# Performance work log

Hardware: AMD Instinct MI355X
Metric: run time of the kernel (lower is better)

Reference implementation:

```python
import jax, jax.numpy as jnp
import numpy as np

N_NODES = 100000


def _gcn_norm(src, dst, n_nodes, n_edges):
    # PyG gcn_norm with add_self_loops=False: deg over target (col) index
    ones = jnp.ones((n_edges,), dtype=jnp.float32)
    deg = jax.ops.segment_sum(ones, dst, num_segments=n_nodes)
    dinv = jnp.where(deg > 0, jax.lax.rsqrt(deg), 0.0)
    return dinv[src] * dinv[dst]  # [E]


def _arma_conv(x, src, dst, ew, init_w, root_w, bias, n_nodes):
    # x: [N, Fin]; init_w/root_w: [K, Fin, Fout]; bias: [K, 1, Fout]
    h = jnp.einsum('nf,kfo->kno', x, init_w)          # [K, N, Fout]
    msg = h[:, src, :] * ew[None, :, None]             # [K, E, Fout]
    agg = jax.vmap(lambda m: jax.ops.segment_sum(m, dst, num_segments=n_nodes))(msg)
    out = agg + jnp.einsum('nf,kfo->kno', x, root_w) + bias
    return jax.nn.relu(out).mean(axis=0)               # mean over stacks K


def setup_inputs() -> dict:
    key = jax.random.key(0)
    ks = jax.random.split(key, 8)
    n, e = N_NODES, 3200000
    nfeat, hid, nclass, K = 512, 16, 40, 2
    x = jax.random.normal(ks[0], (n, nfeat), dtype=jnp.float32)
    edge_index = jax.random.randint(ks[1], (2, e), 0, n, dtype=jnp.int32)
    s1 = (1.0 / np.sqrt(nfeat)).astype(np.float32) if isinstance(np.sqrt(nfeat), np.ndarray) else np.float32(1.0 / np.sqrt(nfeat))
    s2 = np.float32(1.0 / np.sqrt(hid))
    iw1 = jax.random.normal(ks[2], (K, nfeat, hid), dtype=jnp.float32) * s1
    rw1 = jax.random.normal(ks[3], (K, nfeat, hid), dtype=jnp.float32) * s1
    b1 = jax.random.normal(ks[4], (K, 1, hid), dtype=jnp.float32) * 0.01
    iw2 = jax.random.normal(ks[5], (K, hid, nclass), dtype=jnp.float32) * s2
    rw2 = jax.random.normal(ks[6], (K, hid, nclass), dtype=jnp.float32) * s2
    b2 = jax.random.normal(ks[7], (K, 1, nclass), dtype=jnp.float32) * 0.01
    return {'x': x, 'edge_index': edge_index, 'iw1': iw1, 'rw1': rw1, 'b1': b1,
            'iw2': iw2, 'rw2': rw2, 'b2': b2}


def reference(x, edge_index, iw1, rw1, b1, iw2, rw2, b2):
    src, dst = edge_index[0], edge_index[1]
    n = N_NODES
    ew = _gcn_norm(src, dst, n, src.shape[0])
    h = _arma_conv(x, src, dst, ew, iw1, rw1, b1, n)   # [N, 16]
    out = _arma_conv(h, src, dst, ew, iw2, rw2, b2, n) # [N, nclass]
    return out
```

## Files before the change

kernel.cpp:

```cpp
#include <hip/hip_runtime.h>


#define TB 256
#define CHA 4096

typedef __attribute__((ext_vector_type(8))) short bf8;
typedef __attribute__((ext_vector_type(4))) float f4;

__device__ inline unsigned short f2bf_rne(float f) {
  unsigned int u = __float_as_uint(f);
  unsigned int r = u + 0x7fffu + ((u >> 16) & 1u);
  return (unsigned short)(r >> 16);
}
__device__ inline float bf2f(unsigned short h) {
  return __uint_as_float(((unsigned int)h) << 16);
}
__device__ inline float bflo(unsigned int u) { return __uint_as_float(u << 16); }
__device__ inline float bfhi(unsigned int u) { return __uint_as_float(u & 0xffff0000u); }
__device__ inline unsigned int bfpack(float lo, float hi) {
  return (unsigned int)f2bf_rne(lo) | ((unsigned int)f2bf_rne(hi) << 16);
}

#define ACC8(v)                                   \
  do {                                            \
    a[0] += bflo((v).x); a[1] += bfhi((v).x);     \
    a[2] += bflo((v).y); a[3] += bfhi((v).y);     \
    a[4] += bflo((v).z); a[5] += bfhi((v).z);     \
    a[6] += bflo((v).w); a[7] += bfhi((v).w);     \
  } while (0)

#define ACC4(v)                                   \
  do {                                            \
    a[0] += bflo((v).x); a[1] += bfhi((v).x);     \
    a[2] += bflo((v).y); a[3] += bfhi((v).y);     \
  } while (0)

__global__ __launch_bounds__(256) void k_init(int* __restrict__ ccur, int cap) {
  ccur[threadIdx.x] = threadIdx.x * cap;
}

__global__ __launch_bounds__(TB) void k_binA(const int* __restrict__ src,
                                             const int* __restrict__ dst,
                                             int* __restrict__ ccur,
                                             unsigned int* __restrict__ epairs,
                                             int E) {
  __shared__ int cnt[256];
  __shared__ int gb[256];
  int tid = threadIdx.x;
  cnt[tid] = 0;
  __syncthreads();
  int e0 = blockIdx.x * CHA;
  int e1 = min(e0 + CHA, E);
  for (int e = e0 + tid; e < e1; e += TB) atomicAdd(&cnt[dst[e] >> 9], 1);
  __syncthreads();
  int c = cnt[tid];
  if (c > 0) gb[tid] = atomicAdd(&ccur[tid], c);
  __syncthreads();
  cnt[tid] = 0;
  __syncthreads();
  for (int e = e0 + tid; e < e1; e += TB) {
    int dv = dst[e];
    int b = dv >> 9;
    int r = atomicAdd(&cnt[b], 1);
    epairs[gb[b] + r] = ((unsigned int)src[e] << 9) | (unsigned int)(dv & 511);
  }
}

__global__ __launch_bounds__(TB) void k_binB(const unsigned int* __restrict__ epairs,
                                             const int* __restrict__ ccur,
                                             int* __restrict__ degi,
                                             int* __restrict__ offsets,
                                             int* __restrict__ srcs,
                                             float* __restrict__ dinv,
                                             int N, int cap, int scap) {
  __shared__ int cnt[512];
  __shared__ int pre[512];
  int b = blockIdx.x;
  int n0 = b << 9;
  int tid = threadIdx.x;
  int beg = b * cap;
  int end = ccur[b];
  int pbase = b * scap;
  int i0 = tid, i1 = tid + 256;
  cnt[i0] = 0; cnt[i1] = 0;
  __syncthreads();
  for (int e = beg + tid; e < end; e += TB)
    atomicAdd(&cnt[epairs[e] & 511u], 1);
  __syncthreads();
  int pd0 = (cnt[i0] + 7) & ~7;
  int pd1 = (cnt[i1] + 7) & ~7;
  pre[i0] = pd0; pre[i1] = pd1;
  __syncthreads();
  for (int d = 1; d < 512; d <<= 1) {
    int t0 = (i0 >= d) ? pre[i0 - d] : 0;
    int t1 = (i1 >= d) ? pre[i1 - d] : 0;
    __syncthreads();
    pre[i0] += t0; pre[i1] += t1;
    __syncthreads();
  }
  int s0 = pre[i0] - pd0;
  int s1 = pre[i1] - pd1;
  if (n0 + i0 < N) {
    int c0 = cnt[i0];
    degi[n0 + i0] = c0;
    offsets[n0 + i0] = pbase + s0;
    dinv[n0 + i0] = c0 > 0 ? rsqrtf((float)c0) : 0.0f;
  }
  if (n0 + i1 < N) {
    int c1 = cnt[i1];
    degi[n0 + i1] = c1;
    offsets[n0 + i1] = pbase + s1;
    dinv[n0 + i1] = c1 > 0 ? rsqrtf((float)c1) : 0.0f;
  }
  __syncthreads();
  cnt[i0] = s0; cnt[i1] = s1;
  __syncthreads();
  for (int e = beg + tid; e < end; e += TB) {
    unsigned int p = epairs[e];
    int pos = atomicAdd(&cnt[p & 511u], 1);
    srcs[pbase + pos] = (int)(p >> 9);
  }
  __syncthreads();
  for (int j = cnt[i0]; j < pre[i0]; ++j) srcs[pbase + j] = N;
  for (int j = cnt[i1]; j < pre[i1]; ++j) srcs[pbase + j] = N;
}

__global__ __launch_bounds__(TB) void k_wsplit(const float* __restrict__ iw1,
                                               const float* __restrict__ rw1,
                                               short* __restrict__ Whi,
                                               short* __restrict__ Wlo,
                                               unsigned short* __restrict__ Hs,
                                               unsigned short* __restrict__ hs,
                                               int N) {
  int idx = blockIdx.x * TB + threadIdx.x;
  if (idx >= 32768) return;
  if (idx < 32) Hs[(size_t)N * 32 + idx] = 0;
  if (idx < 16) hs[(size_t)N * 16 + idx] = 0;
  int j = idx & 7;
  int l = (idx >> 3) & 63;
  int t = (idx >> 9) & 3;
  int c = idx >> 11;
  int k = c * 32 + (l >> 4) * 8 + j;
  int n = t * 16 + (l & 15);
  float w;
  if (n < 16)
    w = iw1[k * 16 + n];
  else if (n < 32)
    w = iw1[8192 + k * 16 + (n - 16)];
  else if (n < 48)
    w = rw1[k * 16 + (n - 32)];
  else
    w = rw1[8192 + k * 16 + (n - 48)];
  unsigned short h = f2bf_rne(w);
  float res = w - bf2f(h);
  Whi[idx] = (short)h;
  Wlo[idx] = (short)f2bf_rne(res);
}

__global__ __launch_bounds__(TB) void k_gemm1_mfma(const float* __restrict__ x,
                                                   const short* __restrict__ Whi,
                                                   const short* __restrict__ Wlo,
                                                   const float* __restrict__ dinv,
                                                   unsigned short* __restrict__ Hs,
                                                   float* __restrict__ R, int N) {
  int lane = threadIdx.x & 63;
  int wave = threadIdx.x >> 6;
  int row0 = blockIdx.x * 64 + wave * 16;
  int m = lane & 15, quad = lane >> 4;
  int r = row0 + m;
  bool rv = (r < N);
  const float* xr = x + (size_t)r * 512;

  f4 acc[4];
#pragma unroll
  for (int t = 0; t < 4; t++) acc[t] = (f4){0.f, 0.f, 0.f, 0.f};

  for (int c = 0; c < 16; ++c) {
    float xv[8];
    if (rv) {
      f4 a0 = *(const f4*)(xr + c * 32 + quad * 8);
      f4 a1 = *(const f4*)(xr + c * 32 + quad * 8 + 4);
      xv[0] = a0.x; xv[1] = a0.y; xv[2] = a0.z; xv[3] = a0.w;
      xv[4] = a1.x; xv[5] = a1.y; xv[6] = a1.z; xv[7] = a1.w;
    } else {
#pragma unroll
      for (int j = 0; j < 8; ++j) xv[j] = 0.f;
    }
    bf8 ahi, alo;
#pragma unroll
    for (int j = 0; j < 8; ++j) {
      unsigned short h = f2bf_rne(xv[j]);
      float res = xv[j] - bf2f(h);
      ahi[j] = (short)h;
      alo[j] = (short)f2bf_rne(res);
    }
    const short* wb = Whi + ((size_t)(c * 4) * 64 + lane) * 8;
    const short* wl = Wlo + ((size_t)(c * 4) * 64 + lane) * 8;
#pragma unroll
    for (int t = 0; t < 4; ++t) {
      bf8 bh = *(const bf8*)(wb + t * 512);
      bf8 bl = *(const bf8*)(wl + t * 512);
      acc[t] = __builtin_amdgcn_mfma_f32_16x16x32_bf16(ahi, bh, acc[t], 0, 0, 0);
      acc[t] = __builtin_amdgcn_mfma_f32_16x16x32_bf16(alo, bh, acc[t], 0, 0, 0);
      acc[t] = __builtin_amdgcn_mfma_f32_16x16x32_bf16(ahi, bl, acc[t], 0, 0, 0);
    }
  }
  float dv[4];
#pragma unroll
  for (int g = 0; g < 4; ++g) {
    int ro = row0 + quad * 4 + g;
    dv[g] = (ro < N) ? dinv[ro] : 0.f;
  }
#pragma unroll
  for (int t = 0; t < 4; ++t) {
#pragma unroll
    for (int g = 0; g < 4; ++g) {
      int ro = row0 + quad * 4 + g;
      if (ro < N) {
        if (t < 2)
          Hs[(size_t)ro * 32 + t * 16 + m] = f2bf_rne(acc[t][g] * dv[g]);
        else
          R[(size_t)ro * 32 + (t - 2) * 16 + m] = acc[t][g];
      }
    }
  }
}

__global__ __launch_bounds__(TB) void k_prop1(const int* __restrict__ offsets,
                                              const int* __restrict__ degi,
                                              const int* __restrict__ srcs,
                                              const unsigned short* __restrict__ Hs,
                                              const float* __restrict__ R,
                                              const float* __restrict__ dinv,
                                              const float* __restrict__ b1,
                                              float* __restrict__ h,
                                              unsigned short* __restrict__ hs, int N) {
  int tid = blockIdx.x * TB + threadIdx.x;
  int q = tid & 3;
  int n = tid >> 2;
  if (n >= N) return;
  int beg = offsets[n], cnt = degi[n];
  int pdeg = (cnt + 7) & ~7;
  const unsigned short* Hq = Hs + q * 8;
  float a[8];
#pragma unroll
  for (int j = 0; j < 8; j++) a[j] = 0.f;

  if (pdeg) {
    int4 sa = *(const int4*)(srcs + beg);
    int4 sb = *(const int4*)(srcs + beg + 4);
    int i = 0;
    for (; i + 16 <= pdeg; i += 8) {
      uint4 v0 = *(const uint4*)(Hq + (size_t)sa.x * 32);
      uint4 v1 = *(const uint4*)(Hq + (size_t)sa.y * 32);
      uint4 v2 = *(const uint4*)(Hq + (size_t)sa.z * 32);
      uint4 v3 = *(const uint4*)(Hq + (size_t)sa.w * 32);
      uint4 v4 = *(const uint4*)(Hq + (size_t)sb.x * 32);
      uint4 v5 = *(const uint4*)(Hq + (size_t)sb.y * 32);
      uint4 v6 = *(const uint4*)(Hq + (size_t)sb.z * 32);
      uint4 v7 = *(const uint4*)(Hq + (size_t)sb.w * 32);
      sa = *(const int4*)(srcs + beg + i + 8);
      sb = *(const int4*)(srcs + beg + i + 12);
      ACC8(v0); ACC8(v1); ACC8(v2); ACC8(v3);
      ACC8(v4); ACC8(v5); ACC8(v6); ACC8(v7);
    }
    {
      uint4 v0 = *(const uint4*)(Hq + (size_t)sa.x * 32);
      uint4 v1 = *(const uint4*)(Hq + (size_t)sa.y * 32);
      uint4 v2 = *(const uint4*)(Hq + (size_t)sa.z * 32);
      uint4 v3 = *(const uint4*)(Hq + (size_t)sa.w * 32);
      uint4 v4 = *(const uint4*)(Hq + (size_t)sb.x * 32);
      uint4 v5 = *(const uint4*)(Hq + (size_t)sb.y * 32);
      uint4 v6 = *(const uint4*)(Hq + (size_t)sb.z * 32);
      uint4 v7 = *(const uint4*)(Hq + (size_t)sb.w * 32);
      ACC8(v0); ACC8(v1); ACC8(v2); ACC8(v3);
      ACC8(v4); ACC8(v5); ACC8(v6); ACC8(v7);
    }
  }

  float dvn = dinv[n];
  f4 r0 = *(const f4*)(R + (size_t)n * 32 + q * 8);
  f4 r1 = *(const f4*)(R + (size_t)n * 32 + q * 8 + 4);
  float rr[8] = {r0.x, r0.y, r0.z, r0.w, r1.x, r1.y, r1.z, r1.w};
  float vv[8];
#pragma unroll
  for (int j = 0; j < 8; j++) {
    int f = q * 8 + j;
    vv[j] = fmaxf(a[j] * dvn + rr[j] + b1[f], 0.f);
  }
  float pv[8];
#pragma unroll
  for (int j = 0; j < 8; j++) pv[j] = __shfl_xor(vv[j], 2);
  if (q < 2) {
    float hv[8];
#pragma unroll
    for (int j = 0; j < 8; j++) hv[j] = 0.5f * (vv[j] + pv[j]);
    f4 o0 = {hv[0], hv[1], hv[2], hv[3]};
    f4 o1 = {hv[4], hv[5], hv[6], hv[7]};
    *(f4*)(h + (size_t)n * 16 + q * 8) = o0;
    *(f4*)(h + (size_t)n * 16 + q * 8 + 4) = o1;
    uint4 ob;
    ob.x = bfpack(hv[0] * dvn, hv[1] * dvn);
    ob.y = bfpack(hv[2] * dvn, hv[3] * dvn);
    ob.z = bfpack(hv[4] * dvn, hv[5] * dvn);
    ob.w = bfpack(hv[6] * dvn, hv[7] * dvn);
    *(uint4*)(hs + (size_t)n * 16 + q * 8) = ob;
  }
}

__global__ __launch_bounds__(TB) void k_prop2(const int* __restrict__ offsets,
                                              const int* __restrict__ degi,
                                              const int* __restrict__ srcs,
                                              const unsigned short* __restrict__ hs,
                                              const float* __restrict__ dinv,
                                              float* __restrict__ Ah, int N) {
  int tid = blockIdx.x * TB + threadIdx.x;
  int q = tid & 3;
  int n = tid >> 2;
  if (n >= N) return;
  int beg = offsets[n], cnt = degi[n];
  int pdeg = (cnt + 7) & ~7;
  const unsigned short* Hq = hs + q * 4;
  float a[4] = {0.f, 0.f, 0.f, 0.f};

  if (pdeg) {
    int4 sa = *(const int4*)(srcs + beg);
    int4 sb = *(const int4*)(srcs + beg + 4);
    int i = 0;
    for (; i + 16 <= pdeg; i += 8) {
      uint2 v0 = *(const uint2*)(Hq + (size_t)sa.x * 16);
      uint2 v1 = *(const uint2*)(Hq + (size_t)sa.y * 16);
      uint2 v2 = *(const uint2*)(Hq + (size_t)sa.z * 16);
      uint2 v3 = *(const uint2*)(Hq + (size_t)sa.w * 16);
      uint2 v4 = *(const uint2*)(Hq + (size_t)sb.x * 16);
      uint2 v5 = *(const uint2*)(Hq + (size_t)sb.y * 16);
      uint2 v6 = *(const uint2*)(Hq + (size_t)sb.z * 16);
      uint2 v7 = *(const uint2*)(Hq + (size_t)sb.w * 16);
      sa = *(const int4*)(srcs + beg + i + 8);
      sb = *(const int4*)(srcs + beg + i + 12);
      ACC4(v0); ACC4(v1); ACC4(v2); ACC4(v3);
      ACC4(v4); ACC4(v5); ACC4(v6); ACC4(v7);
    }
    {
      uint2 v0 = *(const uint2*)(Hq + (size_t)sa.x * 16);
      uint2 v1 = *(const uint2*)(Hq + (size_t)sa.y * 16);
      uint2 v2 = *(const uint2*)(Hq + (size_t)sa.z * 16);
      uint2 v3 = *(const uint2*)(Hq + (size_t)sa.w * 16);
      uint2 v4 = *(const uint2*)(Hq + (size_t)sb.x * 16);
      uint2 v5 = *(const uint2*)(Hq + (size_t)sb.y * 16);
      uint2 v6 = *(const uint2*)(Hq + (size_t)sb.z * 16);
      uint2 v7 = *(const uint2*)(Hq + (size_t)sb.w * 16);
      ACC4(v0); ACC4(v1); ACC4(v2); ACC4(v3);
      ACC4(v4); ACC4(v5); ACC4(v6); ACC4(v7);
    }
  }

  float dvn = dinv[n];
  f4 o = {a[0] * dvn, a[1] * dvn, a[2] * dvn, a[3] * dvn};
  *(f4*)(Ah + (size_t)n * 16 + q * 4) = o;
}

__global__ __launch_bounds__(TB) void k_final(const float* __restrict__ Ah,
                                              const float* __restrict__ h,
                                              const float* __restrict__ iw2,
                                              const float* __restrict__ rw2,
                                              const float* __restrict__ b2,
                                              float* __restrict__ out, int N) {
  __shared__ float w_iw[2 * 16 * 40];
  __shared__ float w_rw[2 * 16 * 40];
  __shared__ float w_b[2 * 40];
  for (int i = threadIdx.x; i < 1280; i += TB) {
    w_iw[i] = iw2[i];
    w_rw[i] = rw2[i];
  }
  for (int i = threadIdx.x; i < 80; i += TB) w_b[i] = b2[i];
  __syncthreads();

  int idx = blockIdx.x * TB + threadIdx.x;
  if (idx >= N * 40) return;
  int n = idx / 40;
  int o = idx - n * 40;
  float a[16], hr[16];
#pragma unroll
  for (int f = 0; f < 16; f++) {
    a[f] = Ah[(size_t)n * 16 + f];
    hr[f] = h[(size_t)n * 16 + f];
  }
  float res = 0.f;
#pragma unroll
  for (int k = 0; k < 2; k++) {
    float s = w_b[k * 40 + o];
#pragma unroll
    for (int f = 0; f < 16; f++) {
      s += a[f] * w_iw[(k * 16 + f) * 40 + o];
      s += hr[f] * w_rw[(k * 16 + f) * 40 + o];
    }
    res += fmaxf(s, 0.f);
  }
  out[idx] = 0.5f * res;
}

extern "C" void kernel_launch(void* const* d_in, const int* in_sizes, int n_in,
                              void* d_out, int out_size, void* d_ws, size_t ws_size,
                              hipStream_t stream) {
  const float* x = (const float*)d_in[0];
  const int* ei = (const int*)d_in[1];
  const float* iw1 = (const float*)d_in[2];
  const float* rw1 = (const float*)d_in[3];
  const float* b1 = (const float*)d_in[4];
  const float* iw2 = (const float*)d_in[5];
  const float* rw2 = (const float*)d_in[6];
  const float* b2 = (const float*)d_in[7];
  float* out = (float*)d_out;

  const int N = in_sizes[0] / 512;
  const int E = in_sizes[1] / 2;
  const int* src = ei;
  const int* dst = ei + E;
  const int NC = (N + 511) >> 9;

  int mean = (E + NC - 1) / NC;
  int cap = (mean + mean / 8 + 256 + 7) & ~7;
  int scap = cap + 7 * 512;

  char* base = (char*)d_ws;
  size_t off = 0;
  auto alloc = [&](size_t bytes) -> void* {
    off = (off + 255) & ~(size_t)255;
    void* p = base + off;
    off += bytes;
    return p;
  };
  int* degi = (int*)alloc((size_t)N * 4);
  float* dinv = (float*)alloc((size_t)N * 4);
  int* offsets = (int*)alloc((size_t)N * 4);
  int* ccur = (int*)alloc(256 * 4);
  size_t epair_bytes = (size_t)NC * cap * 4;
  size_t r_bytes = (size_t)N * 32 * 4;
  unsigned int* epairs =
      (unsigned int*)alloc(epair_bytes > r_bytes ? epair_bytes : r_bytes);
  int* srcs = (int*)alloc((size_t)NC * scap * 4);
  unsigned short* Hs = (unsigned short*)alloc((size_t)(N + 1) * 32 * 2);
  float* hbuf = (float*)alloc((size_t)N * 16 * 4);
  unsigned short* hs = (unsigned short*)alloc((size_t)(N + 1) * 16 * 2);
  float* Ah = (float*)alloc((size_t)N * 16 * 4);
  short* Whi = (short*)alloc(32768 * 2);
  short* Wlo = (short*)alloc(32768 * 2);
  float* R = (float*)epairs;
  (void)ws_size;

  int NBLK = (E + CHA - 1) / CHA;
  k_init<<<1, 256, 0, stream>>>(ccur, cap);
  k_binA<<<NBLK, TB, 0, stream>>>(src, dst, ccur, epairs, E);
  k_binB<<<NC, TB, 0, stream>>>(epairs, ccur, degi, offsets, srcs, dinv, N, cap, scap);
  k_wsplit<<<128, TB, 0, stream>>>(iw1, rw1, Whi, Wlo, Hs, hs, N);
  k_gemm1_mfma<<<(N + 63) / 64, TB, 0, stream>>>(x, Whi, Wlo, dinv, Hs, R, N);
  int PG = ((size_t)N * 4 + TB - 1) / TB;
  k_prop1<<<PG, TB, 0, stream>>>(offsets, degi, srcs, Hs, R, dinv, b1, hbuf, hs, N);
  k_prop2<<<PG, TB, 0, stream>>>(offsets, degi, srcs, hs, dinv, Ah, N);
  k_final<<<((size_t)N * 40 + TB - 1) / TB, TB, 0, stream>>>(Ah, hbuf, iw2, rw2, b2, out, N);
}
```

Measured before the change: 540.5 us.

## Fuse all stages into one persistent kernel with grid barriers and stage overlap

Replaces the eight separate launches with a single persistent kernel of 1024 blocks that separates stages with software grid barriers built on device-scope atomics. Independent work now runs concurrently: edge binning overlaps the weight split, and the per-bucket CSR build overlaps the MFMA GEMM. The GEMM no longer needs dinv, so it writes unscaled fp32 H1f and a separate pass applies dinv and packs to bf16. This removes launch gaps and serialization between stages, but adds H1f write/read traffic and barrier cost, and it relies on all 1024 blocks being co-resident, otherwise the grid barrier deadlocks.

```diff
diff --git a/kernel.cpp b/kernel.cpp
--- a/kernel.cpp
+++ b/kernel.cpp
@@ -3,6 +3,7 @@
 
 #define TB 256
 #define CHA 4096
+#define NG 1024
 
 typedef __attribute__((ext_vector_type(8))) short bf8;
 typedef __attribute__((ext_vector_type(4))) float f4;
@@ -35,369 +36,353 @@
     a[2] += bflo((v).y); a[3] += bfhi((v).y);     \
   } while (0)
 
-__global__ __launch_bounds__(256) void k_init(int* __restrict__ ccur, int cap) {
-  ccur[threadIdx.x] = threadIdx.x * cap;
-}
-
-__global__ __launch_bounds__(TB) void k_binA(const int* __restrict__ src,
-                                             const int* __restrict__ dst,
-                                             int* __restrict__ ccur,
-                                             unsigned int* __restrict__ epairs,
-                                             int E) {
-  __shared__ int cnt[256];
-  __shared__ int gb[256];
-  int tid = threadIdx.x;
-  cnt[tid] = 0;
+__device__ inline void gbar(int* bar, int G) {
   __syncthreads();
-  int e0 = blockIdx.x * CHA;
-  int e1 = min(e0 + CHA, E);
-  for (int e = e0 + tid; e < e1; e += TB) atomicAdd(&cnt[dst[e] >> 9], 1);
+  __threadfence();
+  if (threadIdx.x == 0) {
+    __hip_atomic_fetch_add(bar, 1, __ATOMIC_ACQ_REL, __HIP_MEMORY_SCOPE_AGENT);
+    while (__hip_atomic_load(bar, __ATOMIC_RELAXED, __HIP_MEMORY_SCOPE_AGENT) < G)
+      __builtin_amdgcn_s_sleep(2);
+  }
   __syncthreads();
-  int c = cnt[tid];
-  if (c > 0) gb[tid] = atomicAdd(&ccur[tid], c);
+  __threadfence();
+}
+
+__global__ __launch_bounds__(TB, 4) void k_mega(
+    const float* __restrict__ x, const int* __restrict__ src,
+    const int* __restrict__ dst, const float* __restrict__ iw1,
+    const float* __restrict__ rw1, const float* __restrict__ b1,
+    const float* __restrict__ iw2, const float* __restrict__ rw2,
+    const float* __restrict__ b2, int* __restrict__ ccur,
+    int* __restrict__ bars, unsigned int* __restrict__ epairs,
+    int* __restrict__ srcs, int* __restrict__ degi, int* __restrict__ offsets,
+    float* __restrict__ dinv, short* __restrict__ Whi, short* __restrict__ Wlo,
+    float* __restrict__ H1f, float* __restrict__ R,
+    unsigned short* __restrict__ Hs, float* __restrict__ hbuf,
+    unsigned short* __restrict__ hs, float* __restrict__ Ah,
+    float* __restrict__ out, int N, int E, int NC, int cap, int scap) {
+  __shared__ union {
+    struct { int cnt[256]; int gb[256]; } ba;
+    struct { int cnt[512]; int pre[512]; } bb;
+    struct { float w_iw[1280]; float w_rw[1280]; float w_b[80]; } fin;
+  } sm;
+
+  const int bid = blockIdx.x;
+  const int tid = threadIdx.x;
+  const int G = gridDim.x;
+  const int NBLK = (E + CHA - 1) / CHA;
+  const int NT = (N + 63) >> 6;
+  const int PG = ((N * 4) + TB - 1) / TB;
+
+  if (bid < NBLK) {
+    sm.ba.cnt[tid] = 0;
+    __syncthreads();
+    int e0 = bid * CHA;
+    int e1 = min(e0 + CHA, E);
+    for (int e = e0 + tid; e < e1; e += TB) atomicAdd(&sm.ba.cnt[dst[e] >> 9], 1);
+    __syncthreads();
+    int c = sm.ba.cnt[tid];
+    if (c > 0) sm.ba.gb[tid] = tid * cap + atomicAdd(&ccur[tid], c);
+    __syncthreads();
+    sm.ba.cnt[tid] = 0;
+    __syncthreads();
+    for (int e = e0 + tid; e < e1; e += TB) {
+      int dv = dst[e];
+      int b = dv >> 9;
+      int r = atomicAdd(&sm.ba.cnt[b], 1);
+      epairs[sm.ba.gb[b] + r] = ((unsigned int)src[e] << 9) | (unsigned int)(dv & 511);
+    }
+  } else {
+    for (int w = bid - NBLK; w < 128; w += G - NBLK) {
+      int idx = w * TB + tid;
+      if (idx < 32) Hs[(size_t)N * 32 + idx] = 0;
+      if (idx < 16) hs[(size_t)N * 16 + idx] = 0;
+      int j = idx & 7;
+      int l = (idx >> 3) & 63;
+      int t = (idx >> 9) & 3;
+      int c = idx >> 11;
+      int k = c * 32 + (l >> 4) * 8 + j;
+      int n = t * 16 + (l & 15);
+      float wv;
+      if (n < 16) wv = iw1[k * 16 + n];
+      else if (n < 32) wv = iw1[8192 + k * 16 + (n - 16)];
+      else if (n < 48) wv = rw1[k * 16 + (n - 32)];
+      else wv = rw1[8192 + k * 16 + (n - 48)];
+      unsigned short hh = f2bf_rne(wv);
+      float res = wv - bf2f(hh);
+      Whi[idx] = (short)hh;
+      Wlo[idx] = (short)f2bf_rne(res);
+    }
+  }
+  gbar(&bars[0], G);
+
+  if (bid < NC) {
+    int b = bid;
+    int n0 = b << 9;
+    int beg = b * cap;
+    int end = beg + ccur[b];
+    int pbase = b * scap;
+    int i0 = tid, i1 = tid + 256;
+    sm.bb.cnt[i0] = 0; sm.bb.cnt[i1] = 0;
+    __syncthreads();
+    for (int e = beg + tid; e < end; e += TB)
+      atomicAdd(&sm.bb.cnt[epairs[e] & 511u], 1);
+    __syncthreads();
+    int pd0 = (sm.bb.cnt[i0] + 7) & ~7;
+    int pd1 = (sm.bb.cnt[i1] + 7) & ~7;
+    sm.bb.pre[i0] = pd0; sm.bb.pre[i1] = pd1;
+    __syncthreads();
+    for (int d = 1; d < 512; d <<= 1) {
+      int t0 = (i0 >= d) ? sm.bb.pre[i0 - d] : 0;
+      int t1 = (i1 >= d) ? sm.bb.pre[i1 - d] : 0;
+      __syncthreads();
+      sm.bb.pre[i0] += t0; sm.bb.pre[i1] += t1;
+      __syncthreads();
+    }
+    int s0 = sm.bb.pre[i0] - pd0;
+    int s1 = sm.bb.pre[i1] - pd1;
+    if (n0 + i0 < N) {
+      int c0 = sm.bb.cnt[i0];
+      degi[n0 + i0] = c0;
+      offsets[n0 + i0] = pbase + s0;
+      dinv[n0 + i0] = c0 > 0 ? rsqrtf((float)c0) : 0.0f;
+    }
+    if (n0 + i1 < N) {
+      int c1 = sm.bb.cnt[i1];
+      degi[n0 + i1] = c1;
+      offsets[n0 + i1] = pbase + s1;
+      dinv[n0 + i1] = c1 > 0 ? rsqrtf((float)c1) : 0.0f;
+    }
+    __syncthreads();
+    sm.bb.cnt[i0] = s0; sm.bb.cnt[i1] = s1;
+    __syncthreads();
+    for (int e = beg + tid; e < end; e += TB) {
+      unsigned int p = epairs[e];
+      int pos = atomicAdd(&sm.bb.cnt[p & 511u], 1);
+      srcs[pbase + pos] = (int)(p >> 9);
+    }
+    __syncthreads();
+    for (int j = sm.bb.cnt[i0]; j < sm.bb.pre[i0]; ++j) srcs[pbase + j] = N;
+    for (int j = sm.bb.cnt[i1]; j < sm.bb.pre[i1]; ++j) srcs[pbase + j] = N;
+  } else {
+    int lane = tid & 63;
+    int wave = tid >> 6;
+    int m = lane & 15, quad = lane >> 4;
+    for (int tile = bid - NC; tile < NT; tile += G - NC) {
+      int row0 = tile * 64 + wave * 16;
+      int r = row0 + m;
+      bool rv = (r < N);
+      const float* xr = x + (size_t)r * 512;
+      f4 acc[4];
+#pragma unroll
+      for (int t = 0; t < 4; t++) acc[t] = (f4){0.f, 0.f, 0.f, 0.f};
+      for (int c = 0; c < 16; ++c) {
+        float xv[8];
+        if (rv) {
+          f4 a0 = *(const f4*)(xr + c * 32 + quad * 8);
+          f4 a1 = *(const f4*)(xr + c * 32 + quad * 8 + 4);
+          xv[0] = a0.x; xv[1] = a0.y; xv[2] = a0.z; xv[3] = a0.w;
+          xv[4] = a1.x; xv[5] = a1.y; xv[6] = a1.z; xv[7] = a1.w;
+        } else {
+#pragma unroll
+          for (int j = 0; j < 8; ++j) xv[j] = 0.f;
+        }
+        bf8 ahi, alo;
+#pragma unroll
+        for (int j = 0; j < 8; ++j) {
+          unsigned short hh = f2bf_rne(xv[j]);
+          float res = xv[j] - bf2f(hh);
+          ahi[j] = (short)hh;
+          alo[j] = (short)f2bf_rne(res);
+        }
+        const short* wb = Whi + ((size_t)(c * 4) * 64 + lane) * 8;
+        const short* wl = Wlo + ((size_t)(c * 4) * 64 + lane) * 8;
+#pragma unroll
+        for (int t = 0; t < 4; ++t) {
+          bf8 bh = *(const bf8*)(wb + t * 512);
+          bf8 bl = *(const bf8*)(wl + t * 512);
+          acc[t] = __builtin_amdgcn_mfma_f32_16x16x32_bf16(ahi, bh, acc[t], 0, 0, 0);
+          acc[t] = __builtin_amdgcn_mfma_f32_16x16x32_bf16(alo, bh, acc[t], 0, 0, 0);
+          acc[t] = __builtin_amdgcn_mfma_f32_16x16x32_bf16(ahi, bl, acc[t], 0, 0, 0);
+        }
+      }
+#pragma unroll
+      for (int t = 0; t < 4; ++t) {
+#pragma unroll
+        for (int g = 0; g < 4; ++g) {
+          int ro = row0 + quad * 4 + g;
+          if (ro < N) {
+            if (t < 2)
+              H1f[(size_t)ro * 32 + t * 16 + m] = acc[t][g];
+            else
+              R[(size_t)ro * 32 + (t - 2) * 16 + m] = acc[t][g];
+          }
+        }
+      }
+    }
+  }
+  gbar(&bars[1], G);
+
+  for (int i = bid * TB + tid; i < N * 4; i += G * TB) {
+    int n = i >> 2;
+    int o = (i & 3) * 8;
+    float d = dinv[n];
+    f4 a0 = *(const f4*)(H1f + (size_t)n * 32 + o);
+    f4 a1 = *(const f4*)(H1f + (size_t)n * 32 + o + 4);
+    uint4 ob;
+    ob.x = bfpack(a0.x * d, a0.y * d);
+    ob.y = bfpack(a0.z * d, a0.w * d);
+    ob.z = bfpack(a1.x * d, a1.y * d);
+    ob.w = bfpack(a1.z * d, a1.w * d);
+    *(uint4*)(Hs + (size_t)n * 32 + o) = ob;
+  }
+  gbar(&bars[2], G);
+
+  for (int g = bid; g < PG; g += G) {
+    int t2 = g * TB + tid;
+    int q = t2 & 3;
+    int n = t2 >> 2;
+    if (n < N) {
+      int beg = offsets[n], cnt = degi[n];
+      int pdeg = (cnt + 7) & ~7;
+      const unsigned short* Hq = Hs + q * 8;
+      float a[8];
+#pragma unroll
+      for (int j = 0; j < 8; j++) a[j] = 0.f;
+      if (pdeg) {
+        int4 sa = *(const int4*)(srcs + beg);
+        int4 sb = *(const int4*)(srcs + beg + 4);
+        int i = 0;
+        for (; i + 16 <= pdeg; i += 8) {
+          uint4 v0 = *(const uint4*)(Hq + (size_t)sa.x * 32);
+          uint4 v1 = *(const uint4*)(Hq + (size_t)sa.y * 32);
+          uint4 v2 = *(const uint4*)(Hq + (size_t)sa.z * 32);
+          uint4 v3 = *(const uint4*)(Hq + (size_t)sa.w * 32);
+          uint4 v4 = *(const uint4*)(Hq + (size_t)sb.x * 32);
+          uint4 v5 = *(const uint4*)(Hq + (size_t)sb.y * 32);
+          uint4 v6 = *(const uint4*)(Hq + (size_t)sb.z * 32);
+          uint4 v7 = *(const uint4*)(Hq + (size_t)sb.w * 32);
+          sa = *(const int4*)(srcs + beg + i + 8);
+          sb = *(const int4*)(srcs + beg + i + 12);
+          ACC8(v0); ACC8(v1); ACC8(v2); ACC8(v3);
+          ACC8(v4); ACC8(v5); ACC8(v6); ACC8(v7);
+        }
+        uint4 v0 = *(const uint4*)(Hq + (size_t)sa.x * 32);
+        uint4 v1 = *(const uint4*)(Hq + (size_t)sa.y * 32);
+        uint4 v2 = *(const uint4*)(Hq + (size_t)sa.z * 32);
+        uint4 v3 = *(const uint4*)(Hq + (size_t)sa.w * 32);
+        uint4 v4 = *(const uint4*)(Hq + (size_t)sb.x * 32);
+        uint4 v5 = *(const uint4*)(Hq + (size_t)sb.y * 32);
+        uint4 v6 = *(const uint4*)(Hq + (size_t)sb.z * 32);
+        uint4 v7 = *(const uint4*)(Hq + (size_t)sb.w * 32);
+        ACC8(v0); ACC8(v1); ACC8(v2); ACC8(v3);
+        ACC8(v4); ACC8(v5); ACC8(v6); ACC8(v7);
+      }
+      float dvn = dinv[n];
+      f4 r0 = *(const f4*)(R + (size_t)n * 32 + q * 8);
+      f4 r1 = *(const f4*)(R + (size_t)n * 32 + q * 8 + 4);
+      float rr[8] = {r0.x, r0.y, r0.z, r0.w, r1.x, r1.y, r1.z, r1.w};
+      float vv[8];
+#pragma unroll
+      for (int j = 0; j < 8; j++) {
+        int f = q * 8 + j;
+        vv[j] = fmaxf(a[j] * dvn + rr[j] + b1[f], 0.f);
+      }
+      float pv[8];
+#pragma unroll
+      for (int j = 0; j < 8; j++) pv[j] = __shfl_xor(vv[j], 2);
+      if (q < 2) {
+        float hv[8];
+#pragma unroll
+        for (int j = 0; j < 8; j++) hv[j] = 0.5f * (vv[j] + pv[j]);
+        f4 o0 = {hv[0], hv[1], hv[2], hv[3]};
+        f4 o1 = {hv[4], hv[5], hv[6], hv[7]};
+        *(f4*)(hbuf + (size_t)n * 16 + q * 8) = o0;
+        *(f4*)(hbuf + (size_t)n * 16 + q * 8 + 4) = o1;
+        uint4 ob;
+        ob.x = bfpack(hv[0] * dvn, hv[1] * dvn);
+        ob.y = bfpack(hv[2] * dvn, hv[3] * dvn);
+        ob.z = bfpack(hv[4] * dvn, hv[5] * dvn);
+        ob.w = bfpack(hv[6] * dvn, hv[7] * dvn);
+        *(uint4*)(hs + (size_t)n * 16 + q * 8) = ob;
+      }
+    }
+  }
+  gbar(&bars[3], G);
+
+  for (int g = bid; g < PG; g += G) {
+    int t2 = g * TB + tid;
+    int q = t2 & 3;
+    int n = t2 >> 2;
+    if (n < N) {
+      int beg = offsets[n], cnt = degi[n];
+      int pdeg = (cnt + 7) & ~7;
+      const unsigned short* Hq = hs + q * 4;
+      float a[4] = {0.f, 0.f, 0.f, 0.f};
+      if (pdeg) {
+        int4 sa = *(const int4*)(srcs + beg);
+        int4 sb = *(const int4*)(srcs + beg + 4);
+        int i = 0;
+        for (; i + 16 <= pdeg; i += 8) {
+          uint2 v0 = *(const uint2*)(Hq + (size_t)sa.x * 16);
+          uint2 v1 = *(const uint2*)(Hq + (size_t)sa.y * 16);
+          uint2 v2 = *(const uint2*)(Hq + (size_t)sa.z * 16);
+          uint2 v3 = *(const uint2*)(Hq + (size_t)sa.w * 16);
+          uint2 v4 = *(const uint2*)(Hq + (size_t)sb.x * 16);
+          uint2 v5 = *(const uint2*)(Hq + (size_t)sb.y * 16);
+          uint2 v6 = *(const uint2*)(Hq + (size_t)sb.z * 16);
+          uint2 v7 = *(const uint2*)(Hq + (size_t)sb.w * 16);
+          sa = *(const int4*)(srcs + beg + i + 8);
+          sb = *(const int4*)(srcs + beg + i + 12);
+          ACC4(v0); ACC4(v1); ACC4(v2); ACC4(v3);
+          ACC4(v4); ACC4(v5); ACC4(v6); ACC4(v7);
+        }
+        uint2 v0 = *(const uint2*)(Hq + (size_t)sa.x * 16);
+        uint2 v1 = *(const uint2*)(Hq + (size_t)sa.y * 16);
+        uint2 v2 = *(const uint2*)(Hq + (size_t)sa.z * 16);
+        uint2 v3 = *(const uint2*)(Hq + (size_t)sa.w * 16);
+        uint2 v4 = *(const uint2*)(Hq + (size_t)sb.x * 16);
+        uint2 v5 = *(const uint2*)(Hq + (size_t)sb.y * 16);
+        uint2 v6 = *(const uint2*)(Hq + (size_t)sb.z * 16);
+        uint2 v7 = *(const uint2*)(Hq + (size_t)sb.w * 16);
+        ACC4(v0); ACC4(v1); ACC4(v2); ACC4(v3);
+        ACC4(v4); ACC4(v5); ACC4(v6); ACC4(v7);
+      }
+      float dvn = dinv[n];
+      f4 o = {a[0] * dvn, a[1] * dvn, a[2] * dvn, a[3] * dvn};
+      *(f4*)(Ah + (size_t)n * 16 + q * 4) = o;
+    }
+  }
+  gbar(&bars[4], G);
+
+  for (int i = tid; i < 1280; i += TB) {
+    sm.fin.w_iw[i] = iw2[i];
+    sm.fin.w_rw[i] = rw2[i];
+  }
+  for (int i = tid; i < 80; i += TB) sm.fin.w_b[i] = b2[i];
   __syncthreads();
-  cnt[tid] = 0;
-  __syncthreads();
-  for (int e = e0 + tid; e < e1; e += TB) {
-    int dv = dst[e];
-    int b = dv >> 9;
-    int r = atomicAdd(&cnt[b], 1);
-    epairs[gb[b] + r] = ((unsigned int)src[e] << 9) | (unsigned int)(dv & 511);
-  }
-}
-
-__global__ __launch_bounds__(TB) void k_binB(const unsigned int* __restrict__ epairs,
-                                             const int* __restrict__ ccur,
-                                             int* __restrict__ degi,
-                                             int* __restrict__ offsets,
-                                             int* __restrict__ srcs,
-                                             float* __restrict__ dinv,
-                                             int N, int cap, int scap) {
-  __shared__ int cnt[512];
-  __shared__ int pre[512];
-  int b = blockIdx.x;
-  int n0 = b << 9;
-  int tid = threadIdx.x;
-  int beg = b * cap;
-  int end = ccur[b];
-  int pbase = b * scap;
-  int i0 = tid, i1 = tid + 256;
-  cnt[i0] = 0; cnt[i1] = 0;
-  __syncthreads();
-  for (int e = beg + tid; e < end; e += TB)
-    atomicAdd(&cnt[epairs[e] & 511u], 1);
-  __syncthreads();
-  int pd0 = (cnt[i0] + 7) & ~7;
-  int pd1 = (cnt[i1] + 7) & ~7;
-  pre[i0] = pd0; pre[i1] = pd1;
-  __syncthreads();
-  for (int d = 1; d < 512; d <<= 1) {
-    int t0 = (i0 >= d) ? pre[i0 - d] : 0;
-    int t1 = (i1 >= d) ? pre[i1 - d] : 0;
-    __syncthreads();
-    pre[i0] += t0; pre[i1] += t1;
-    __syncthreads();
-  }
-  int s0 = pre[i0] - pd0;
-  int s1 = pre[i1] - pd1;
-  if (n0 + i0 < N) {
-    int c0 = cnt[i0];
-    degi[n0 + i0] = c0;
-    offsets[n0 + i0] = pbase + s0;
-    dinv[n0 + i0] = c0 > 0 ? rsqrtf((float)c0) : 0.0f;
-  }
-  if (n0 + i1 < N) {
-    int c1 = cnt[i1];
-    degi[n0 + i1] = c1;
-    offsets[n0 + i1] = pbase + s1;
-    dinv[n0 + i1] = c1 > 0 ? rsqrtf((float)c1) : 0.0f;
-  }
-  __syncthreads();
-  cnt[i0] = s0; cnt[i1] = s1;
-  __syncthreads();
-  for (int e = beg + tid; e < end; e += TB) {
-    unsigned int p = epairs[e];
-    int pos = atomicAdd(&cnt[p & 511u], 1);
-    srcs[pbase + pos] = (int)(p >> 9);
-  }
-  __syncthreads();
-  for (int j = cnt[i0]; j < pre[i0]; ++j) srcs[pbase + j] = N;
-  for (int j = cnt[i1]; j < pre[i1]; ++j) srcs[pbase + j] = N;
-}
-
-__global__ __launch_bounds__(TB) void k_wsplit(const float* __restrict__ iw1,
-                                               const float* __restrict__ rw1,
-                                               short* __restrict__ Whi,
-                                               short* __restrict__ Wlo,
-                                               unsigned short* __restrict__ Hs,
-                                               unsigned short* __restrict__ hs,
-                                               int N) {
-  int idx = blockIdx.x * TB + threadIdx.x;
-  if (idx >= 32768) return;
-  if (idx < 32) Hs[(size_t)N * 32 + idx] = 0;
-  if (idx < 16) hs[(size_t)N * 16 + idx] = 0;
-  int j = idx & 7;
-  int l = (idx >> 3) & 63;
-  int t = (idx >> 9) & 3;
-  int c = idx >> 11;
-  int k = c * 32 + (l >> 4) * 8 + j;
-  int n = t * 16 + (l & 15);
-  float w;
-  if (n < 16)
-    w = iw1[k * 16 + n];
-  else if (n < 32)
-    w = iw1[8192 + k * 16 + (n - 16)];
-  else if (n < 48)
-    w = rw1[k * 16 + (n - 32)];
-  else
-    w = rw1[8192 + k * 16 + (n - 48)];
-  unsigned short h = f2bf_rne(w);
-  float res = w - bf2f(h);
-  Whi[idx] = (short)h;
-  Wlo[idx] = (short)f2bf_rne(res);
-}
-
-__global__ __launch_bounds__(TB) void k_gemm1_mfma(const float* __restrict__ x,
-                                                   const short* __restrict__ Whi,
-                                                   const short* __restrict__ Wlo,
-                                                   const float* __restrict__ dinv,
-                                                   unsigned short* __restrict__ Hs,
-                                                   float* __restrict__ R, int N) {
-  int lane = threadIdx.x & 63;
-  int wave = threadIdx.x >> 6;
-  int row0 = blockIdx.x * 64 + wave * 16;
-  int m = lane & 15, quad = lane >> 4;
-  int r = row0 + m;
-  bool rv = (r < N);
-  const float* xr = x + (size_t)r * 512;
-
-  f4 acc[4];
-#pragma unroll
-  for (int t = 0; t < 4; t++) acc[t] = (f4){0.f, 0.f, 0.f, 0.f};
-
-  for (int c = 0; c < 16; ++c) {
-    float xv[8];
-    if (rv) {
-      f4 a0 = *(const f4*)(xr + c * 32 + quad * 8);
-      f4 a1 = *(const f4*)(xr + c * 32 + quad * 8 + 4);
-      xv[0] = a0.x; xv[1] = a0.y; xv[2] = a0.z; xv[3] = a0.w;
-      xv[4] = a1.x; xv[5] = a1.y; xv[6] = a1.z; xv[7] = a1.w;
-    } else {
-#pragma unroll
-      for (int j = 0; j < 8; ++j) xv[j] = 0.f;
-    }
-    bf8 ahi, alo;
-#pragma unroll
-    for (int j = 0; j < 8; ++j) {
-      unsigned short h = f2bf_rne(xv[j]);
-      float res = xv[j] - bf2f(h);
-      ahi[j] = (short)h;
-      alo[j] = (short)f2bf_rne(res);
-    }
-    const short* wb = Whi + ((size_t)(c * 4) * 64 + lane) * 8;
-    const short* wl = Wlo + ((size_t)(c * 4) * 64 + lane) * 8;
-#pragma unroll
-    for (int t = 0; t < 4; ++t) {
-      bf8 bh = *(const bf8*)(wb + t * 512);
-      bf8 bl = *(const bf8*)(wl + t * 512);
-      acc[t] = __builtin_amdgcn_mfma_f32_16x16x32_bf16(ahi, bh, acc[t], 0, 0, 0);
-      acc[t] = __builtin_amdgcn_mfma_f32_16x16x32_bf16(alo, bh, acc[t], 0, 0, 0);
-      acc[t] = __builtin_amdgcn_mfma_f32_16x16x32_bf16(ahi, bl, acc[t], 0, 0, 0);
-    }
-  }
-  float dv[4];
-#pragma unroll
-  for (int g = 0; g < 4; ++g) {
-    int ro = row0 + quad * 4 + g;
-    dv[g] = (ro < N) ? dinv[ro] : 0.f;
-  }
-#pragma unroll
-  for (int t = 0; t < 4; ++t) {
-#pragma unroll
-    for (int g = 0; g < 4; ++g) {
-      int ro = row0 + quad * 4 + g;
-      if (ro < N) {
-        if (t < 2)
-          Hs[(size_t)ro * 32 + t * 16 + m] = f2bf_rne(acc[t][g] * dv[g]);
-        else
-          R[(size_t)ro * 32 + (t - 2) * 16 + m] = acc[t][g];
-      }
-    }
-  }
-}
-
-__global__ __launch_bounds__(TB) void k_prop1(const int* __restrict__ offsets,
-                                              const int* __restrict__ degi,
-                                              const int* __restrict__ srcs,
-                                              const unsigned short* __restrict__ Hs,
-                                              const float* __restrict__ R,
-                                              const float* __restrict__ dinv,
-                                              const float* __restrict__ b1,
-                                              float* __restrict__ h,
-                                              unsigned short* __restrict__ hs, int N) {
-  int tid = blockIdx.x * TB + threadIdx.x;
-  int q = tid & 3;
-  int n = tid >> 2;
-  if (n >= N) return;
-  int beg = offsets[n], cnt = degi[n];
-  int pdeg = (cnt + 7) & ~7;
-  const unsigned short* Hq = Hs + q * 8;
-  float a[8];
-#pragma unroll
-  for (int j = 0; j < 8; j++) a[j] = 0.f;
-
-  if (pdeg) {
-    int4 sa = *(const int4*)(srcs + beg);
-    int4 sb = *(const int4*)(srcs + beg + 4);
-    int i = 0;
-    for (; i + 16 <= pdeg; i += 8) {
-      uint4 v0 = *(const uint4*)(Hq + (size_t)sa.x * 32);
-      uint4 v1 = *(const uint4*)(Hq + (size_t)sa.y * 32);
-      uint4 v2 = *(const uint4*)(Hq + (size_t)sa.z * 32);
-      uint4 v3 = *(const uint4*)(Hq + (size_t)sa.w * 32);
-      uint4 v4 = *(const uint4*)(Hq + (size_t)sb.x * 32);
-      uint4 v5 = *(const uint4*)(Hq + (size_t)sb.y * 32);
-      uint4 v6 = *(const uint4*)(Hq + (size_t)sb.z * 32);
-      uint4 v7 = *(const uint4*)(Hq + (size_t)sb.w * 32);
-      sa = *(const int4*)(srcs + beg + i + 8);
-      sb = *(const int4*)(srcs + beg + i + 12);
-      ACC8(v0); ACC8(v1); ACC8(v2); ACC8(v3);
-      ACC8(v4); ACC8(v5); ACC8(v6); ACC8(v7);
-    }
-    {
-      uint4 v0 = *(const uint4*)(Hq + (size_t)sa.x * 32);
-      uint4 v1 = *(const uint4*)(Hq + (size_t)sa.y * 32);
-      uint4 v2 = *(const uint4*)(Hq + (size_t)sa.z * 32);
-      uint4 v3 = *(const uint4*)(Hq + (size_t)sa.w * 32);
-      uint4 v4 = *(const uint4*)(Hq + (size_t)sb.x * 32);
-      uint4 v5 = *(const uint4*)(Hq + (size_t)sb.y * 32);
-      uint4 v6 = *(const uint4*)(Hq + (size_t)sb.z * 32);
-      uint4 v7 = *(const uint4*)(Hq + (size_t)sb.w * 32);
-      ACC8(v0); ACC8(v1); ACC8(v2); ACC8(v3);
-      ACC8(v4); ACC8(v5); ACC8(v6); ACC8(v7);
-    }
-  }
-
-  float dvn = dinv[n];
-  f4 r0 = *(const f4*)(R + (size_t)n * 32 + q * 8);
-  f4 r1 = *(const f4*)(R + (size_t)n * 32 + q * 8 + 4);
-  float rr[8] = {r0.x, r0.y, r0.z, r0.w, r1.x, r1.y, r1.z, r1.w};
-  float vv[8];
-#pragma unroll
-  for (int j = 0; j < 8; j++) {
-    int f = q * 8 + j;
-    vv[j] = fmaxf(a[j] * dvn + rr[j] + b1[f], 0.f);
-  }
-  float pv[8];
-#pragma unroll
-  for (int j = 0; j < 8; j++) pv[j] = __shfl_xor(vv[j], 2);
-  if (q < 2) {
-    float hv[8];
-#pragma unroll
-    for (int j = 0; j < 8; j++) hv[j] = 0.5f * (vv[j] + pv[j]);
-    f4 o0 = {hv[0], hv[1], hv[2], hv[3]};
-    f4 o1 = {hv[4], hv[5], hv[6], hv[7]};
-    *(f4*)(h + (size_t)n * 16 + q * 8) = o0;
-    *(f4*)(h + (size_t)n * 16 + q * 8 + 4) = o1;
-    uint4 ob;
-    ob.x = bfpack(hv[0] * dvn, hv[1] * dvn);
-    ob.y = bfpack(hv[2] * dvn, hv[3] * dvn);
-    ob.z = bfpack(hv[4] * dvn, hv[5] * dvn);
-    ob.w = bfpack(hv[6] * dvn, hv[7] * dvn);
-    *(uint4*)(hs + (size_t)n * 16 + q * 8) = ob;
-  }
-}
-
-__global__ __launch_bounds__(TB) void k_prop2(const int* __restrict__ offsets,
-                                              const int* __restrict__ degi,
-                                              const int* __restrict__ srcs,
-                                              const unsigned short* __restrict__ hs,
-                                              const float* __restrict__ dinv,
-                                              float* __restrict__ Ah, int N) {
-  int tid = blockIdx.x * TB + threadIdx.x;
-  int q = tid & 3;
-  int n = tid >> 2;
-  if (n >= N) return;
-  int beg = offsets[n], cnt = degi[n];
-  int pdeg = (cnt + 7) & ~7;
-  const unsigned short* Hq = hs + q * 4;
-  float a[4] = {0.f, 0.f, 0.f, 0.f};
-
-  if (pdeg) {
-    int4 sa = *(const int4*)(srcs + beg);
-    int4 sb = *(const int4*)(srcs + beg + 4);
-    int i = 0;
-    for (; i + 16 <= pdeg; i += 8) {
-      uint2 v0 = *(const uint2*)(Hq + (size_t)sa.x * 16);
-      uint2 v1 = *(const uint2*)(Hq + (size_t)sa.y * 16);
-      uint2 v2 = *(const uint2*)(Hq + (size_t)sa.z * 16);
-      uint2 v3 = *(const uint2*)(Hq + (size_t)sa.w * 16);
-      uint2 v4 = *(const uint2*)(Hq + (size_t)sb.x * 16);
-      uint2 v5 = *(const uint2*)(Hq + (size_t)sb.y * 16);
-      uint2 v6 = *(const uint2*)(Hq + (size_t)sb.z * 16);
-      uint2 v7 = *(const uint2*)(Hq + (size_t)sb.w * 16);
-      sa = *(const int4*)(srcs + beg + i + 8);
-      sb = *(const int4*)(srcs + beg + i + 12);
-      ACC4(v0); ACC4(v1); ACC4(v2); ACC4(v3);
-      ACC4(v4); ACC4(v5); ACC4(v6); ACC4(v7);
-    }
-    {
-      uint2 v0 = *(const uint2*)(Hq + (size_t)sa.x * 16);
-      uint2 v1 = *(const uint2*)(Hq + (size_t)sa.y * 16);
-      uint2 v2 = *(const uint2*)(Hq + (size_t)sa.z * 16);
-      uint2 v3 = *(const uint2*)(Hq + (size_t)sa.w * 16);
-      uint2 v4 = *(const uint2*)(Hq + (size_t)sb.x * 16);
-      uint2 v5 = *(const uint2*)(Hq + (size_t)sb.y * 16);
-      uint2 v6 = *(const uint2*)(Hq + (size_t)sb.z * 16);
-      uint2 v7 = *(const uint2*)(Hq + (size_t)sb.w * 16);
-      ACC4(v0); ACC4(v1); ACC4(v2); ACC4(v3);
-      ACC4(v4); ACC4(v5); ACC4(v6); ACC4(v7);
-    }
-  }
-
-  float dvn = dinv[n];
-  f4 o = {a[0] * dvn, a[1] * dvn, a[2] * dvn, a[3] * dvn};
-  *(f4*)(Ah + (size_t)n * 16 + q * 4) = o;
-}
-
-__global__ __launch_bounds__(TB) void k_final(const float* __restrict__ Ah,
-                                              const float* __restrict__ h,
-                                              const float* __restrict__ iw2,
-                                              const float* __restrict__ rw2,
-                                              const float* __restrict__ b2,
-                                              float* __restrict__ out, int N) {
-  __shared__ float w_iw[2 * 16 * 40];
-  __shared__ float w_rw[2 * 16 * 40];
-  __shared__ float w_b[2 * 40];
-  for (int i = threadIdx.x; i < 1280; i += TB) {
-    w_iw[i] = iw2[i];
-    w_rw[i] = rw2[i];
-  }
-  for (int i = threadIdx.x; i < 80; i += TB) w_b[i] = b2[i];
-  __syncthreads();
-
-  int idx = blockIdx.x * TB + threadIdx.x;
-  if (idx >= N * 40) return;
-  int n = idx / 40;
-  int o = idx - n * 40;
-  float a[16], hr[16];
-#pragma unroll
-  for (int f = 0; f < 16; f++) {
-    a[f] = Ah[(size_t)n * 16 + f];
-    hr[f] = h[(size_t)n * 16 + f];
-  }
-  float res = 0.f;
-#pragma unroll
-  for (int k = 0; k < 2; k++) {
-    float s = w_b[k * 40 + o];
+  for (int idx = bid * TB + tid; idx < N * 40; idx += G * TB) {
+    int n = idx / 40;
+    int o = idx - n * 40;
+    float a[16], hr[16];
 #pragma unroll
     for (int f = 0; f < 16; f++) {
-      s += a[f] * w_iw[(k * 16 + f) * 40 + o];
-      s += hr[f] * w_rw[(k * 16 + f) * 40 + o];
-    }
-    res += fmaxf(s, 0.f);
-  }
-  out[idx] = 0.5f * res;
+      a[f] = Ah[(size_t)n * 16 + f];
+      hr[f] = hbuf[(size_t)n * 16 + f];
+    }
+    float res = 0.f;
+#pragma unroll
+    for (int k = 0; k < 2; k++) {
+      float s = sm.fin.w_b[k * 40 + o];
+#pragma unroll
+      for (int f = 0; f < 16; f++) {
+        s += a[f] * sm.fin.w_iw[(k * 16 + f) * 40 + o];
+        s += hr[f] * sm.fin.w_rw[(k * 16 + f) * 40 + o];
+      }
+      res += fmaxf(s, 0.f);
+    }
+    out[idx] = 0.5f * res;
+  }
 }
 
 extern "C" void kernel_launch(void* const* d_in, const int* in_sizes, int n_in,
@@ -434,29 +419,24 @@
   int* degi = (int*)alloc((size_t)N * 4);
   float* dinv = (float*)alloc((size_t)N * 4);
   int* offsets = (int*)alloc((size_t)N * 4);
-  int* ccur = (int*)alloc(256 * 4);
-  size_t epair_bytes = (size_t)NC * cap * 4;
-  size_t r_bytes = (size_t)N * 32 * 4;
-  unsigned int* epairs =
-      (unsigned int*)alloc(epair_bytes > r_bytes ? epair_bytes : r_bytes);
+  int* cz = (int*)alloc(264 * 4);
+  int* ccur = cz;
+  int* bars = cz + 256;
+  unsigned int* epairs = (unsigned int*)alloc((size_t)NC * cap * 4);
   int* srcs = (int*)alloc((size_t)NC * scap * 4);
   unsigned short* Hs = (unsigned short*)alloc((size_t)(N + 1) * 32 * 2);
+  float* H1f = (float*)alloc((size_t)N * 32 * 4);
+  float* R = (float*)alloc((size_t)N * 32 * 4);
   float* hbuf = (float*)alloc((size_t)N * 16 * 4);
   unsigned short* hs = (unsigned short*)alloc((size_t)(N + 1) * 16 * 2);
   float* Ah = (float*)alloc((size_t)N * 16 * 4);
   short* Whi = (short*)alloc(32768 * 2);
   short* Wlo = (short*)alloc(32768 * 2);
-  float* R = (float*)epairs;
   (void)ws_size;
 
-  int NBLK = (E + CHA - 1) / CHA;
-  k_init<<<1, 256, 0, stream>>>(ccur, cap);
-  k_binA<<<NBLK, TB, 0, stream>>>(src, dst, ccur, epairs, E);
-  k_binB<<<NC, TB, 0, stream>>>(epairs, ccur, degi, offsets, srcs, dinv, N, cap, scap);
-  k_wsplit<<<128, TB, 0, stream>>>(iw1, rw1, Whi, Wlo, Hs, hs, N);
-  k_gemm1_mfma<<<(N + 63) / 64, TB, 0, stream>>>(x, Whi, Wlo, dinv, Hs, R, N);
-  int PG = ((size_t)N * 4 + TB - 1) / TB;
-  k_prop1<<<PG, TB, 0, stream>>>(offsets, degi, srcs, Hs, R, dinv, b1, hbuf, hs, N);
-  k_prop2<<<PG, TB, 0, stream>>>(offsets, degi, srcs, hs, dinv, Ah, N);
-  k_final<<<((size_t)N * 40 + TB - 1) / TB, TB, 0, stream>>>(Ah, hbuf, iw2, rw2, b2, out, N);
-}
+  hipMemsetAsync(cz, 0, 264 * 4, stream);
+  k_mega<<<NG, TB, 0, stream>>>(x, src, dst, iw1, rw1, b1, iw2, rw2, b2,
+                                ccur, bars, epairs, srcs, degi, offsets, dinv,
+                                Whi, Wlo, H1f, R, Hs, hbuf, hs, Ah, out,
+                                N, E, NC, cap, scap);
+}
```

Measured after the change: 1.764 ms. 3.26x slower.
